# Kernel tuning notes

Hardware: AMD Instinct MI355X
Metric: run time of the kernel (lower is better)

Reference implementation:

```python
import jax, jax.numpy as jnp
import numpy as np

N_NODES = 50000
N_EDGES = 800000
IN_DIM = 128
HID = 128
N_GRAPHS = 1024


def gcn_conv(x, W, b, src, dst, n_nodes):
    # PyG GCNConv: add self-loops, symmetric normalization, aggregate at dst, then bias.
    loop = jnp.arange(n_nodes, dtype=src.dtype)
    s = jnp.concatenate([src, loop])
    d = jnp.concatenate([dst, loop])
    deg = jax.ops.segment_sum(jnp.ones_like(d, dtype=x.dtype), d, num_segments=n_nodes)
    dinv = jnp.where(deg > 0, deg ** -0.5, 0.0)
    norm = dinv[s] * dinv[d]                      # [E+N]
    h = x @ W                                     # [N, out]
    msg = h[s] * norm[:, None]                    # gather + scale
    out = jax.ops.segment_sum(msg, d, num_segments=n_nodes)  # scatter-add
    return out + b


def setup_inputs() -> dict:
    key = jax.random.key(0)
    ks = jax.random.split(key, 10)
    x = jax.random.normal(ks[0], (N_NODES, IN_DIM), dtype=jnp.float32)
    src = jax.random.randint(ks[1], (N_EDGES,), 0, N_NODES, dtype=jnp.int32)
    dst = jax.random.randint(ks[2], (N_EDGES,), 0, N_NODES, dtype=jnp.int32)
    batch = jnp.sort(jax.random.randint(ks[3], (N_NODES,), 0, N_GRAPHS, dtype=jnp.int32))
    sc1 = 1.0 / np.sqrt(IN_DIM)
    sc2 = 1.0 / np.sqrt(HID)
    W1 = jax.random.uniform(ks[4], (IN_DIM, HID), jnp.float32, -sc1, sc1)
    b1 = jnp.zeros((HID,), jnp.float32)
    W2 = jax.random.uniform(ks[5], (HID, HID), jnp.float32, -sc2, sc2)
    b2 = jnp.zeros((HID,), jnp.float32)
    Wlin = jax.random.uniform(ks[6], (HID, 1), jnp.float32, -sc2, sc2)
    blin = jnp.zeros((1,), jnp.float32)
    return {"x": x, "src": src, "dst": dst, "batch": batch, "n_graphs": N_GRAPHS,
            "W1": W1, "b1": b1, "W2": W2, "b2": b2, "Wlin": Wlin, "blin": blin}


def reference(x, src, dst, batch, n_graphs, W1, b1, W2, b2, Wlin, blin):
    n = x.shape[0]
    h = jax.nn.relu(gcn_conv(x, W1, b1, src, dst, n))
    h = jax.nn.relu(gcn_conv(h, W2, b2, src, dst, n))
    # global_mean_pool over graph assignment
    summed = jax.ops.segment_sum(h, batch, num_segments=n_graphs)
    cnt = jax.ops.segment_sum(jnp.ones((n,), h.dtype), batch, num_segments=n_graphs)
    pooled = summed / jnp.maximum(cnt, 1.0)[:, None]
    return (pooled @ Wlin + blin).reshape(-1)
```

## Files before the change

kernel.cpp:

```cpp
#include <hip/hip_runtime.h>
#include <hip/hip_bf16.h>

#define DIM 128
typedef unsigned int u32;

typedef __attribute__((ext_vector_type(8))) short bf16x8;
typedef __attribute__((ext_vector_type(4))) float f32x4;
typedef __attribute__((ext_vector_type(2))) float f32x2;

__device__ __forceinline__ u32 pack_bf16x2(float a, float b) {
    u32 ua = __float_as_uint(a), ub = __float_as_uint(b);
    ua = (ua + 0x7FFFu + ((ua >> 16) & 1u)) >> 16;
    ub = (ub + 0x7FFFu + ((ub >> 16) & 1u)) >> 16;
    return ua | (ub << 16);
}
__device__ __forceinline__ float2 unpack_bf16x2(u32 h) {
    return make_float2(__uint_as_float(h << 16), __uint_as_float(h & 0xFFFF0000u));
}

#if __has_builtin(__builtin_amdgcn_cvt_pk_f32_fp8) && __has_builtin(__builtin_amdgcn_cvt_pk_fp8_f32)
#define FP8_HW 1
#endif

__device__ __forceinline__ void dec4(float* d, u32 w) {
#ifdef FP8_HW
    f32x2 a = __builtin_amdgcn_cvt_pk_f32_fp8((int)w, false);
    f32x2 b = __builtin_amdgcn_cvt_pk_f32_fp8((int)w, true);
    d[0] = a.x; d[1] = a.y; d[2] = b.x; d[3] = b.y;
#else
    #pragma unroll
    for (int i = 0; i < 4; ++i) {
        u32 v = (w >> (8 * i)) & 0xFFu;
        u32 s = v >> 7, e = (v >> 3) & 15u, m = v & 7u;
        float nv = __uint_as_float((s << 31) | ((e + 120u) << 23) | (m << 20));
        float sv = (s ? -1.f : 1.f) * (float)m * 0.001953125f;
        d[i] = e ? nv : sv;
    }
#endif
}

#ifndef FP8_HW
__device__ __forceinline__ u32 enc_byte(float f) {
    u32 s = __float_as_uint(f) >> 31;
    float af = fminf(fabsf(f), 448.f);
    u32 b;
    if (af >= 0.015625f) {
        u32 m = __float_as_uint(af);
        m = m + 0x0007FFFFu + ((m >> 20) & 1u);
        u32 fe = (m >> 23) - 120u;
        if (fe > 15u) b = (15u << 3) | 6u;
        else          b = (fe << 3) | ((m >> 20) & 7u);
    } else {
        b = (u32)rintf(af * 512.f);
    }
    return b | (s << 7);
}
#endif

template<bool HI>
__device__ __forceinline__ u32 enc_pair(float a, float b, u32 old) {
#ifdef FP8_HW
    return (u32)__builtin_amdgcn_cvt_pk_fp8_f32(a, b, (int)old, HI);
#else
    u32 p = enc_byte(a) | (enc_byte(b) << 8);
    return HI ? ((old & 0x0000FFFFu) | (p << 16)) : ((old & 0xFFFF0000u) | p);
#endif
}

__device__ __forceinline__ void addrow8(float* acc, uint2 r) {
    float d[4];
    dec4(d, r.x);
    acc[0] += d[0]; acc[1] += d[1]; acc[2] += d[2]; acc[3] += d[3];
    dec4(d, r.y);
    acc[4] += d[0]; acc[5] += d[1]; acc[6] += d[2]; acc[7] += d[3];
}

__global__ void count_rank(int* __restrict__ deg, const int* __restrict__ dst,
                           int* __restrict__ rank, int* __restrict__ total, int E)
{
    int e = blockIdx.x * blockDim.x + threadIdx.x;
    if (e == 0) *total = 0;
    if (e < E) rank[e] = atomicAdd(&deg[dst[e]], 1);
}

__global__ __launch_bounds__(256) void alloc_offsets(
    const int* __restrict__ deg, int* __restrict__ start, int* __restrict__ endp,
    float* __restrict__ dinv, int* __restrict__ total,
    int* __restrict__ csr, int N,
    float* __restrict__ sums, float* __restrict__ cnt, int G,
    u32* __restrict__ B0, u32* __restrict__ B1)
{
    int i = blockIdx.x * blockDim.x + threadIdx.x;
    int lane = threadIdx.x & 63;
    if (i < G) { sums[i] = 0.f; cnt[i] = 0.f; }
    if (i < 32) {
        B0[(size_t)N * 32 + i] = 0u;
        B1[(size_t)N * 32 + i] = 0u;
    }
    int d  = (i < N) ? deg[i] : 0;
    int d4 = (d + 3) & ~3;
    int pre = d4;
    #pragma unroll
    for (int off = 1; off < 64; off <<= 1) {
        int v = __shfl_up(pre, off, 64);
        if (lane >= off) pre += v;
    }
    int waveTot = __shfl(pre, 63, 64);
    int base = 0;
    if (lane == 63) base = atomicAdd(total, waveTot);
    base = __shfl(base, 63, 64);
    if (i < N) {
        int st = base + pre - d4;
        start[i] = st;
        endp[i]  = st + d4;
        dinv[i]  = rsqrtf((float)(d + 1));
        for (int p = d; p < d4; ++p)
            csr[st + p] = N;
    }
}

__device__ __forceinline__ void gemm_body0(
    const float* __restrict__ X, const float* __restrict__ W,
    const float* __restrict__ dinv, u32* __restrict__ Y, int N,
    int tile0, int tstride)
{
    __shared__ u32   Abuf[16][68];
    __shared__ float Dbuf[16][132];

    const int t    = threadIdx.x;
    const int grp  = t >> 4;
    const int gl   = t & 15;
    const int lane = t & 63;
    const int wv   = t >> 6;
    const int lrow = lane & 15;
    const int lhi  = lane >> 4;

    bf16x8 bfr[2][4];
    {
        const float* wp = W + (size_t)(lhi * 8) * DIM + wv * 32 + lrow;
        #pragma unroll
        for (int nt = 0; nt < 2; ++nt)
            #pragma unroll
            for (int kc = 0; kc < 4; ++kc) {
                const float* p = wp + (size_t)(kc * 32) * DIM + nt * 16;
                union { u32 u[4]; bf16x8 v; } tmp;
                #pragma unroll
                for (int e = 0; e < 4; ++e)
                    tmp.u[e] = pack_bf16x2(p[(size_t)(2 * e) * DIM],
                                           p[(size_t)(2 * e + 1) * DIM]);
                bfr[nt][kc] = tmp.v;
            }
    }

    const int ntiles = (N + 15) >> 4;
    for (int tile = tile0; tile < ntiles; tile += tstride) {
        const int node = tile * 16 + grp;
        const bool valid = node < N;

        float4 a0 = make_float4(0.f, 0.f, 0.f, 0.f);
        float4 a1 = make_float4(0.f, 0.f, 0.f, 0.f);
        if (valid) {
            a0 = *(const float4*)&X[(size_t)node * DIM + gl * 8];
            a1 = *(const float4*)&X[(size_t)node * DIM + gl * 8 + 4];
        }
        uint4 pk;
        pk.x = pack_bf16x2(a0.x, a0.y);
        pk.y = pack_bf16x2(a0.z, a0.w);
        pk.z = pack_bf16x2(a1.x, a1.y);
        pk.w = pack_bf16x2(a1.z, a1.w);
        *(uint4*)&Abuf[grp][gl * 4] = pk;
        __syncthreads();

        f32x4 c0 = {0.f, 0.f, 0.f, 0.f};
        f32x4 c1 = {0.f, 0.f, 0.f, 0.f};
        #pragma unroll
        for (int kc = 0; kc < 4; ++kc) {
            bf16x8 afr = *(const bf16x8*)&Abuf[lrow][kc * 16 + lhi * 4];
            c0 = __builtin_amdgcn_mfma_f32_16x16x32_bf16(afr, bfr[0][kc], c0, 0, 0, 0);
            c1 = __builtin_amdgcn_mfma_f32_16x16x32_bf16(afr, bfr[1][kc], c1, 0, 0, 0);
        }
        #pragma unroll
        for (int r = 0; r < 4; ++r) {
            Dbuf[lhi * 4 + r][wv * 32 + lrow]      = c0[r];
            Dbuf[lhi * 4 + r][wv * 32 + 16 + lrow] = c1[r];
        }
        __syncthreads();

        if (valid) {
            float dnp = 16.f * dinv[node];
            float4 o0 = *(const float4*)&Dbuf[grp][gl * 8];
            float4 o1 = *(const float4*)&Dbuf[grp][gl * 8 + 4];
            u32 lo = enc_pair<false>(dnp * o0.x, dnp * o0.y, 0u);
            lo     = enc_pair<true >(dnp * o0.z, dnp * o0.w, lo);
            u32 hi = enc_pair<false>(dnp * o1.x, dnp * o1.y, 0u);
            hi     = enc_pair<true >(dnp * o1.z, dnp * o1.w, hi);
            *(uint2*)&Y[(size_t)node * 32 + gl * 2] = make_uint2(lo, hi);
        }
    }
}

__global__ __launch_bounds__(256) void scatter_gemm1(
    const float* __restrict__ x, const float* __restrict__ W1,
    const float* __restrict__ dinv, u32* __restrict__ Y, int N, int gblocks,
    const int* __restrict__ src, const int* __restrict__ dst,
    const int* __restrict__ rank, const int* __restrict__ start,
    int* __restrict__ csr, int E)
{
    if ((int)blockIdx.x < gblocks) {
        gemm_body0(x, W1, dinv, Y, N, blockIdx.x, gblocks);
    } else {
        int e = ((int)blockIdx.x - gblocks) * 256 + threadIdx.x;
        if (e < E) {
            int d = dst[e];
            csr[start[d] + rank[e]] = src[e];
        }
    }
}

__device__ __forceinline__ void gather_core8(
    const u32* __restrict__ Hl, const int* __restrict__ csr,
    int st, int en_pad, float* acc)
{
    int j = st;
    for (; j + 8 <= en_pad; j += 8) {
        int4 sa = *(const int4*)&csr[j];
        int4 sb = *(const int4*)&csr[j + 4];
        uint2 r0 = *(const uint2*)&Hl[(size_t)sa.x * 32];
        uint2 r1 = *(const uint2*)&Hl[(size_t)sa.y * 32];
        uint2 r2 = *(const uint2*)&Hl[(size_t)sa.z * 32];
        uint2 r3 = *(const uint2*)&Hl[(size_t)sa.w * 32];
        uint2 r4 = *(const uint2*)&Hl[(size_t)sb.x * 32];
        uint2 r5 = *(const uint2*)&Hl[(size_t)sb.y * 32];
        uint2 r6 = *(const uint2*)&Hl[(size_t)sb.z * 32];
        uint2 r7 = *(const uint2*)&Hl[(size_t)sb.w * 32];
        addrow8(acc, r0); addrow8(acc, r1); addrow8(acc, r2); addrow8(acc, r3);
        addrow8(acc, r4); addrow8(acc, r5); addrow8(acc, r6); addrow8(acc, r7);
    }
    if (j < en_pad) {
        int4 sa = *(const int4*)&csr[j];
        uint2 r0 = *(const uint2*)&Hl[(size_t)sa.x * 32];
        uint2 r1 = *(const uint2*)&Hl[(size_t)sa.y * 32];
        uint2 r2 = *(const uint2*)&Hl[(size_t)sa.z * 32];
        uint2 r3 = *(const uint2*)&Hl[(size_t)sa.w * 32];
        addrow8(acc, r0); addrow8(acc, r1); addrow8(acc, r2); addrow8(acc, r3);
    }
}

__global__ __launch_bounds__(256) void gather_gemm(
    const u32* __restrict__ H, u32* __restrict__ O,
    const int* __restrict__ csr, const int* __restrict__ start,
    const int* __restrict__ endp, const float* __restrict__ dinv, int N,
    const float* __restrict__ b1, const float* __restrict__ W2)
{
    __shared__ u32   Abuf[16][68];
    __shared__ float Dbuf[16][132];

    const int t    = threadIdx.x;
    const int grp  = t >> 4;
    const int gl   = t & 15;
    const int node = blockIdx.x * 16 + grp;
    const bool valid = node < N;

    const int lane = t & 63;
    const int wv   = t >> 6;
    const int lrow = lane & 15;
    const int lhi  = lane >> 4;

    bf16x8 bfr[2][4];
    {
        const float* wp = W2 + (size_t)(lhi * 8) * DIM + wv * 32 + lrow;
        #pragma unroll
        for (int nt = 0; nt < 2; ++nt)
            #pragma unroll
            for (int kc = 0; kc < 4; ++kc) {
                const float* p = wp + (size_t)(kc * 32) * DIM + nt * 16;
                union { u32 u[4]; bf16x8 v; } tmp;
                #pragma unroll
                for (int e = 0; e < 4; ++e)
                    tmp.u[e] = pack_bf16x2(p[(size_t)(2 * e) * DIM],
                                           p[(size_t)(2 * e + 1) * DIM]);
                bfr[nt][kc] = tmp.v;
            }
    }

    float acc[8] = {0.f,0.f,0.f,0.f,0.f,0.f,0.f,0.f};
    float dn = 0.f;
    if (valid) {
        const u32* Hl = H + gl * 2;
        gather_core8(Hl, csr, start[node], endp[node], acc);
        addrow8(acc, *(const uint2*)&Hl[(size_t)node * 32]);
        dn = dinv[node] * 0.0625f;
    }

    {
        int f0 = gl * 8;
        float4 bA = *(const float4*)&b1[f0];
        float4 bB = *(const float4*)&b1[f0 + 4];
        float bb[8] = {bA.x,bA.y,bA.z,bA.w,bB.x,bB.y,bB.z,bB.w};
        float r[8];
        #pragma unroll
        for (int i = 0; i < 8; ++i)
            r[i] = fmaxf(fmaf(dn, acc[i], bb[i]), 0.f);
        uint4 pk;
        pk.x = pack_bf16x2(r[0], r[1]);
        pk.y = pack_bf16x2(r[2], r[3]);
        pk.z = pack_bf16x2(r[4], r[5]);
        pk.w = pack_bf16x2(r[6], r[7]);
        *(uint4*)&Abuf[grp][gl * 4] = pk;
    }
    __syncthreads();

    f32x4 c0 = {0.f, 0.f, 0.f, 0.f};
    f32x4 c1 = {0.f, 0.f, 0.f, 0.f};
    #pragma unroll
    for (int kc = 0; kc < 4; ++kc) {
        bf16x8 afr = *(const bf16x8*)&Abuf[lrow][kc * 16 + lhi * 4];
        c0 = __builtin_amdgcn_mfma_f32_16x16x32_bf16(afr, bfr[0][kc], c0, 0, 0, 0);
        c1 = __builtin_amdgcn_mfma_f32_16x16x32_bf16(afr, bfr[1][kc], c1, 0, 0, 0);
    }

    #pragma unroll
    for (int r = 0; r < 4; ++r) {
        Dbuf[lhi * 4 + r][wv * 32 + lrow]      = c0[r];
        Dbuf[lhi * 4 + r][wv * 32 + 16 + lrow] = c1[r];
    }
    __syncthreads();

    if (valid) {
        float dnp = 16.f * dinv[node];
        float4 o0 = *(const float4*)&Dbuf[grp][gl * 8];
        float4 o1 = *(const float4*)&Dbuf[grp][gl * 8 + 4];
        u32 lo = enc_pair<false>(dnp * o0.x, dnp * o0.y, 0u);
        lo     = enc_pair<true >(dnp * o0.z, dnp * o0.w, lo);
        u32 hi = enc_pair<false>(dnp * o1.x, dnp * o1.y, 0u);
        hi     = enc_pair<true >(dnp * o1.z, dnp * o1.w, hi);
        *(uint2*)&O[(size_t)node * 32 + gl * 2] = make_uint2(lo, hi);
    }
}

__global__ __launch_bounds__(256) void gather_pool(
    const u32* __restrict__ H,
    const int* __restrict__ csr, const int* __restrict__ start,
    const int* __restrict__ endp, const float* __restrict__ dinv, int N,
    const float* __restrict__ b2, const float* __restrict__ wlin,
    const int* __restrict__ batch, float* __restrict__ sums, float* __restrict__ cnt)
{
    const int grp  = threadIdx.x >> 4;
    const int gl   = threadIdx.x & 15;
    const int node = blockIdx.x * 16 + grp;
    if (node >= N) return;

    float acc[8] = {0.f,0.f,0.f,0.f,0.f,0.f,0.f,0.f};
    const u32* Hl = H + gl * 2;
    gather_core8(Hl, csr, start[node], endp[node], acc);
    addrow8(acc, *(const uint2*)&Hl[(size_t)node * 32]);
    float dn = dinv[node] * 0.0625f;

    int f0 = gl * 8;
    float v = 0.f;
    #pragma unroll
    for (int i = 0; i < 8; ++i)
        v += fmaxf(fmaf(dn, acc[i], b2[f0 + i]), 0.f) * wlin[f0 + i];
    #pragma unroll
    for (int m = 1; m <= 8; m <<= 1) v += __shfl_xor(v, m, 64);
    if (gl == 0) {
        int g = batch[node];
        unsafeAtomicAdd(&sums[g], v);
        unsafeAtomicAdd(&cnt[g], 1.0f);
    }
}

__global__ void final_kernel(const float* __restrict__ sums,
                             const float* __restrict__ cnt,
                             const float* __restrict__ blin,
                             float* __restrict__ out, int G)
{
    int g = blockIdx.x * blockDim.x + threadIdx.x;
    if (g < G) out[g] = sums[g] / fmaxf(cnt[g], 1.0f) + blin[0];
}


extern "C" void kernel_launch(void* const* d_in, const int* in_sizes, int n_in,
                              void* d_out, int out_size, void* d_ws, size_t ws_size,
                              hipStream_t stream)
{
    const float* x    = (const float*)d_in[0];
    const int*   src  = (const int*)d_in[1];
    const int*   dst  = (const int*)d_in[2];
    const int*   batch= (const int*)d_in[3];
    const float* W1   = (const float*)d_in[5];
    const float* b1   = (const float*)d_in[6];
    const float* W2   = (const float*)d_in[7];
    const float* b2   = (const float*)d_in[8];
    const float* wlin = (const float*)d_in[9];
    const float* blin = (const float*)d_in[10];
    float* out = (float*)d_out;

    const int N = in_sizes[0] / DIM;
    const int E = in_sizes[1];
    const int G = out_size;
    const size_t E_pad = (size_t)E + 4 * (size_t)N;

    u32*   B0    = (u32*)d_ws;
    u32*   B1    = B0 + (size_t)(N + 1) * 32;
    float* dinv  = (float*)(B1 + (size_t)(N + 1) * 32);
    float* sums  = dinv + N;
    float* cnt   = sums + G;
    int*   deg_c = (int*)(cnt + G);
    int*   start = deg_c + N;
    int*   endp  = start + N;
    int*   rank  = endp + N;
    int*   csr   = rank + E;
    int*   total = csr + E_pad;
    size_t need_bytes = ((size_t)(total + 1) - (size_t)d_ws);
    if (ws_size < need_bytes) return;

    const int eblocks  = (E + 255) / 256;
    const int g4blocks = (N + 15) / 16;
    const int g1blocks = g4blocks < 1024 ? g4blocks : 1024;

    (void)hipMemsetAsync(deg_c, 0, sizeof(int) * (size_t)N, stream);
    count_rank<<<eblocks, 256, 0, stream>>>(deg_c, dst, rank, total, E);
    alloc_offsets<<<(N + 255) / 256, 256, 0, stream>>>(deg_c, start, endp,
                                                       dinv, total, csr, N,
                                                       sums, cnt, G, B0, B1);
    scatter_gemm1<<<g1blocks + eblocks, 256, 0, stream>>>(x, W1, dinv, B0, N,
                                                          g1blocks, src, dst,
                                                          rank, start, csr, E);
    gather_gemm<<<g4blocks, 256, 0, stream>>>(B0, B1, csr, start, endp, dinv,
                                              N, b1, W2);
    gather_pool<<<g4blocks, 256, 0, stream>>>(B1, csr, start, endp, dinv, N,
                                              b2, wlin, batch, sums, cnt);
    final_kernel<<<(G + 255) / 256, 256, 0, stream>>>(sums, cnt, blin, out, G);
}
```

Measured before the change: 245.2 us.

## Gather 16 fp8 features per thread and prefetch next CSR indices

The gather kernels now use 8 threads per node instead of 16. Each thread loads 16 fp8 features per neighbor as one 16-byte load, and each block covers 32 nodes. The gather loop is restructured to prefetch the next 8 CSR indices while the current neighbor rows are being loaded. The GEMM stage runs two MFMA halves over the 32-node tile. The goal is fewer, wider memory transactions and less index-load latency, at the cost of twice the accumulator registers and a halved thread count per node.

```diff
diff --git a/kernel.cpp b/kernel.cpp
--- a/kernel.cpp
+++ b/kernel.cpp
@@ -67,12 +67,16 @@
 #endif
 }
 
-__device__ __forceinline__ void addrow8(float* acc, uint2 r) {
+__device__ __forceinline__ void addrow16(float* acc, uint4 r) {
     float d[4];
     dec4(d, r.x);
-    acc[0] += d[0]; acc[1] += d[1]; acc[2] += d[2]; acc[3] += d[3];
+    acc[0]  += d[0]; acc[1]  += d[1]; acc[2]  += d[2]; acc[3]  += d[3];
     dec4(d, r.y);
-    acc[4] += d[0]; acc[5] += d[1]; acc[6] += d[2]; acc[7] += d[3];
+    acc[4]  += d[0]; acc[5]  += d[1]; acc[6]  += d[2]; acc[7]  += d[3];
+    dec4(d, r.z);
+    acc[8]  += d[0]; acc[9]  += d[1]; acc[10] += d[2]; acc[11] += d[3];
+    dec4(d, r.w);
+    acc[12] += d[0]; acc[13] += d[1]; acc[14] += d[2]; acc[15] += d[3];
 }
 
 __global__ void count_rank(int* __restrict__ deg, const int* __restrict__ dst,
@@ -217,32 +221,47 @@
     }
 }
 
-__device__ __forceinline__ void gather_core8(
+__device__ __forceinline__ void gather_core16(
     const u32* __restrict__ Hl, const int* __restrict__ csr,
-    int st, int en_pad, float* acc)
+    int st, int en, float* acc)
 {
     int j = st;
-    for (; j + 8 <= en_pad; j += 8) {
+    if (j + 8 <= en) {
         int4 sa = *(const int4*)&csr[j];
         int4 sb = *(const int4*)&csr[j + 4];
-        uint2 r0 = *(const uint2*)&Hl[(size_t)sa.x * 32];
-        uint2 r1 = *(const uint2*)&Hl[(size_t)sa.y * 32];
-        uint2 r2 = *(const uint2*)&Hl[(size_t)sa.z * 32];
-        uint2 r3 = *(const uint2*)&Hl[(size_t)sa.w * 32];
-        uint2 r4 = *(const uint2*)&Hl[(size_t)sb.x * 32];
-        uint2 r5 = *(const uint2*)&Hl[(size_t)sb.y * 32];
-        uint2 r6 = *(const uint2*)&Hl[(size_t)sb.z * 32];
-        uint2 r7 = *(const uint2*)&Hl[(size_t)sb.w * 32];
-        addrow8(acc, r0); addrow8(acc, r1); addrow8(acc, r2); addrow8(acc, r3);
-        addrow8(acc, r4); addrow8(acc, r5); addrow8(acc, r6); addrow8(acc, r7);
-    }
-    if (j < en_pad) {
+        while (true) {
+            int jn = j + 8;
+            bool next8 = (jn + 8 <= en);
+            int4 na, nb;
+            if (next8) {
+                na = *(const int4*)&csr[jn];
+                nb = *(const int4*)&csr[jn + 4];
+            }
+            uint4 r0 = *(const uint4*)&Hl[(size_t)sa.x * 32];
+            uint4 r1 = *(const uint4*)&Hl[(size_t)sa.y * 32];
+            uint4 r2 = *(const uint4*)&Hl[(size_t)sa.z * 32];
+            uint4 r3 = *(const uint4*)&Hl[(size_t)sa.w * 32];
+            uint4 r4 = *(const uint4*)&Hl[(size_t)sb.x * 32];
+            uint4 r5 = *(const uint4*)&Hl[(size_t)sb.y * 32];
+            uint4 r6 = *(const uint4*)&Hl[(size_t)sb.z * 32];
+            uint4 r7 = *(const uint4*)&Hl[(size_t)sb.w * 32];
+            addrow16(acc, r0); addrow16(acc, r1);
+            addrow16(acc, r2); addrow16(acc, r3);
+            addrow16(acc, r4); addrow16(acc, r5);
+            addrow16(acc, r6); addrow16(acc, r7);
+            j = jn;
+            if (!next8) break;
+            sa = na; sb = nb;
+        }
+    }
+    if (j < en) {
         int4 sa = *(const int4*)&csr[j];
-        uint2 r0 = *(const uint2*)&Hl[(size_t)sa.x * 32];
-        uint2 r1 = *(const uint2*)&Hl[(size_t)sa.y * 32];
-        uint2 r2 = *(const uint2*)&Hl[(size_t)sa.z * 32];
-        uint2 r3 = *(const uint2*)&Hl[(size_t)sa.w * 32];
-        addrow8(acc, r0); addrow8(acc, r1); addrow8(acc, r2); addrow8(acc, r3);
+        uint4 r0 = *(const uint4*)&Hl[(size_t)sa.x * 32];
+        uint4 r1 = *(const uint4*)&Hl[(size_t)sa.y * 32];
+        uint4 r2 = *(const uint4*)&Hl[(size_t)sa.z * 32];
+        uint4 r3 = *(const uint4*)&Hl[(size_t)sa.w * 32];
+        addrow16(acc, r0); addrow16(acc, r1);
+        addrow16(acc, r2); addrow16(acc, r3);
     }
 }
 
@@ -252,13 +271,13 @@
     const int* __restrict__ endp, const float* __restrict__ dinv, int N,
     const float* __restrict__ b1, const float* __restrict__ W2)
 {
-    __shared__ u32   Abuf[16][68];
-    __shared__ float Dbuf[16][132];
+    __shared__ u32   Abuf[32][68];
+    __shared__ float Dbuf[32][132];
 
     const int t    = threadIdx.x;
-    const int grp  = t >> 4;
-    const int gl   = t & 15;
-    const int node = blockIdx.x * 16 + grp;
+    const int grp  = t >> 3;
+    const int gl   = t & 7;
+    const int node = blockIdx.x * 32 + grp;
     const bool valid = node < N;
 
     const int lane = t & 63;
@@ -283,58 +302,75 @@
             }
     }
 
-    float acc[8] = {0.f,0.f,0.f,0.f,0.f,0.f,0.f,0.f};
+    float acc[16];
+    #pragma unroll
+    for (int i = 0; i < 16; ++i) acc[i] = 0.f;
     float dn = 0.f;
     if (valid) {
-        const u32* Hl = H + gl * 2;
-        gather_core8(Hl, csr, start[node], endp[node], acc);
-        addrow8(acc, *(const uint2*)&Hl[(size_t)node * 32]);
+        const u32* Hl = H + gl * 4;
+        gather_core16(Hl, csr, start[node], endp[node], acc);
+        addrow16(acc, *(const uint4*)&Hl[(size_t)node * 32]);
         dn = dinv[node] * 0.0625f;
     }
 
     {
-        int f0 = gl * 8;
-        float4 bA = *(const float4*)&b1[f0];
-        float4 bB = *(const float4*)&b1[f0 + 4];
-        float bb[8] = {bA.x,bA.y,bA.z,bA.w,bB.x,bB.y,bB.z,bB.w};
-        float r[8];
-        #pragma unroll
-        for (int i = 0; i < 8; ++i)
-            r[i] = fmaxf(fmaf(dn, acc[i], bb[i]), 0.f);
-        uint4 pk;
-        pk.x = pack_bf16x2(r[0], r[1]);
-        pk.y = pack_bf16x2(r[2], r[3]);
-        pk.z = pack_bf16x2(r[4], r[5]);
-        pk.w = pack_bf16x2(r[6], r[7]);
-        *(uint4*)&Abuf[grp][gl * 4] = pk;
+        int f0 = gl * 16;
+        float r[16];
+        #pragma unroll
+        for (int i = 0; i < 16; i += 4) {
+            float4 bb = *(const float4*)&b1[f0 + i];
+            r[i]     = fmaxf(fmaf(dn, acc[i],     bb.x), 0.f);
+            r[i + 1] = fmaxf(fmaf(dn, acc[i + 1], bb.y), 0.f);
+            r[i + 2] = fmaxf(fmaf(dn, acc[i + 2], bb.z), 0.f);
+            r[i + 3] = fmaxf(fmaf(dn, acc[i + 3], bb.w), 0.f);
+        }
+        uint4 p0, p1;
+        p0.x = pack_bf16x2(r[0],  r[1]);
+        p0.y = pack_bf16x2(r[2],  r[3]);
+        p0.z = pack_bf16x2(r[4],  r[5]);
+        p0.w = pack_bf16x2(r[6],  r[7]);
+        p1.x = pack_bf16x2(r[8],  r[9]);
+        p1.y = pack_bf16x2(r[10], r[11]);
+        p1.z = pack_bf16x2(r[12], r[13]);
+        p1.w = pack_bf16x2(r[14], r[15]);
+        *(uint4*)&Abuf[grp][gl * 8]     = p0;
+        *(uint4*)&Abuf[grp][gl * 8 + 4] = p1;
     }
     __syncthreads();
 
-    f32x4 c0 = {0.f, 0.f, 0.f, 0.f};
-    f32x4 c1 = {0.f, 0.f, 0.f, 0.f};
-    #pragma unroll
-    for (int kc = 0; kc < 4; ++kc) {
-        bf16x8 afr = *(const bf16x8*)&Abuf[lrow][kc * 16 + lhi * 4];
-        c0 = __builtin_amdgcn_mfma_f32_16x16x32_bf16(afr, bfr[0][kc], c0, 0, 0, 0);
-        c1 = __builtin_amdgcn_mfma_f32_16x16x32_bf16(afr, bfr[1][kc], c1, 0, 0, 0);
-    }
-
-    #pragma unroll
-    for (int r = 0; r < 4; ++r) {
-        Dbuf[lhi * 4 + r][wv * 32 + lrow]      = c0[r];
-        Dbuf[lhi * 4 + r][wv * 32 + 16 + lrow] = c1[r];
+    #pragma unroll
+    for (int half = 0; half < 2; ++half) {
+        f32x4 c0 = {0.f, 0.f, 0.f, 0.f};
+        f32x4 c1 = {0.f, 0.f, 0.f, 0.f};
+        #pragma unroll
+        for (int kc = 0; kc < 4; ++kc) {
+            bf16x8 afr = *(const bf16x8*)&Abuf[half * 16 + lrow][kc * 16 + lhi * 4];
+            c0 = __builtin_amdgcn_mfma_f32_16x16x32_bf16(afr, bfr[0][kc], c0, 0, 0, 0);
+            c1 = __builtin_amdgcn_mfma_f32_16x16x32_bf16(afr, bfr[1][kc], c1, 0, 0, 0);
+        }
+        #pragma unroll
+        for (int r = 0; r < 4; ++r) {
+            Dbuf[half * 16 + lhi * 4 + r][wv * 32 + lrow]      = c0[r];
+            Dbuf[half * 16 + lhi * 4 + r][wv * 32 + 16 + lrow] = c1[r];
+        }
     }
     __syncthreads();
 
     if (valid) {
         float dnp = 16.f * dinv[node];
-        float4 o0 = *(const float4*)&Dbuf[grp][gl * 8];
-        float4 o1 = *(const float4*)&Dbuf[grp][gl * 8 + 4];
-        u32 lo = enc_pair<false>(dnp * o0.x, dnp * o0.y, 0u);
-        lo     = enc_pair<true >(dnp * o0.z, dnp * o0.w, lo);
-        u32 hi = enc_pair<false>(dnp * o1.x, dnp * o1.y, 0u);
-        hi     = enc_pair<true >(dnp * o1.z, dnp * o1.w, hi);
-        *(uint2*)&O[(size_t)node * 32 + gl * 2] = make_uint2(lo, hi);
+        float o[16];
+        #pragma unroll
+        for (int i = 0; i < 16; ++i) o[i] = Dbuf[grp][gl * 16 + i];
+        uint4 ov;
+        ov.x = enc_pair<true>(dnp * o[2],  dnp * o[3],
+               enc_pair<false>(dnp * o[0],  dnp * o[1],  0u));
+        ov.y = enc_pair<true>(dnp * o[6],  dnp * o[7],
+               enc_pair<false>(dnp * o[4],  dnp * o[5],  0u));
+        ov.z = enc_pair<true>(dnp * o[10], dnp * o[11],
+               enc_pair<false>(dnp * o[8],  dnp * o[9],  0u));
+        ov.w = enc_pair<true>(dnp * o[14], dnp * o[15],
+               enc_pair<false>(dnp * o[12], dnp * o[13], 0u));
+        *(uint4*)&O[(size_t)node * 32 + gl * 4] = ov;
     }
 }
 
@@ -345,24 +381,33 @@
     const float* __restrict__ b2, const float* __restrict__ wlin,
     const int* __restrict__ batch, float* __restrict__ sums, float* __restrict__ cnt)
 {
-    const int grp  = threadIdx.x >> 4;
-    const int gl   = threadIdx.x & 15;
-    const int node = blockIdx.x * 16 + grp;
+    const int grp  = threadIdx.x >> 3;
+    const int gl   = threadIdx.x & 7;
+    const int node = blockIdx.x * 32 + grp;
     if (node >= N) return;
 
-    float acc[8] = {0.f,0.f,0.f,0.f,0.f,0.f,0.f,0.f};
-    const u32* Hl = H + gl * 2;
-    gather_core8(Hl, csr, start[node], endp[node], acc);
-    addrow8(acc, *(const uint2*)&Hl[(size_t)node * 32]);
+    float acc[16];
+    #pragma unroll
+    for (int i = 0; i < 16; ++i) acc[i] = 0.f;
+    const u32* Hl = H + gl * 4;
+    gather_core16(Hl, csr, start[node], endp[node], acc);
+    addrow16(acc, *(const uint4*)&Hl[(size_t)node * 32]);
     float dn = dinv[node] * 0.0625f;
 
-    int f0 = gl * 8;
+    int f0 = gl * 16;
     float v = 0.f;
     #pragma unroll
-    for (int i = 0; i < 8; ++i)
-        v += fmaxf(fmaf(dn, acc[i], b2[f0 + i]), 0.f) * wlin[f0 + i];
-    #pragma unroll
-    for (int m = 1; m <= 8; m <<= 1) v += __shfl_xor(v, m, 64);
+    for (int i = 0; i < 16; i += 4) {
+        float4 bb = *(const float4*)&b2[f0 + i];
+        float4 ww = *(const float4*)&wlin[f0 + i];
+        v += fmaxf(fmaf(dn, acc[i],     bb.x), 0.f) * ww.x;
+        v += fmaxf(fmaf(dn, acc[i + 1], bb.y), 0.f) * ww.y;
+        v += fmaxf(fmaf(dn, acc[i + 2], bb.z), 0.f) * ww.z;
+        v += fmaxf(fmaf(dn, acc[i + 3], bb.w), 0.f) * ww.w;
+    }
+    v += __shfl_xor(v, 1, 64);
+    v += __shfl_xor(v, 2, 64);
+    v += __shfl_xor(v, 4, 64);
     if (gl == 0) {
         int g = batch[node];
         unsafeAtomicAdd(&sums[g], v);
@@ -418,6 +463,7 @@
     const int eblocks  = (E + 255) / 256;
     const int g4blocks = (N + 15) / 16;
     const int g1blocks = g4blocks < 1024 ? g4blocks : 1024;
+    const int g32blocks = (N + 31) / 32;
 
     (void)hipMemsetAsync(deg_c, 0, sizeof(int) * (size_t)N, stream);
     count_rank<<<eblocks, 256, 0, stream>>>(deg_c, dst, rank, total, E);
@@ -427,9 +473,9 @@
     scatter_gemm1<<<g1blocks + eblocks, 256, 0, stream>>>(x, W1, dinv, B0, N,
                                                           g1blocks, src, dst,
                                                           rank, start, csr, E);
-    gather_gemm<<<g4blocks, 256, 0, stream>>>(B0, B1, csr, start, endp, dinv,
-                                              N, b1, W2);
-    gather_pool<<<g4blocks, 256, 0, stream>>>(B1, csr, start, endp, dinv, N,
-                                              b2, wlin, batch, sums, cnt);
+    gather_gemm<<<g32blocks, 256, 0, stream>>>(B0, B1, csr, start, endp, dinv,
+                                               N, b1, W2);
+    gather_pool<<<g32blocks, 256, 0, stream>>>(B1, csr, start, endp, dinv, N,
+                                               b2, wlin, batch, sums, cnt);
     final_kernel<<<(G + 255) / 256, 256, 0, stream>>>(sums, cnt, blin, out, G);
 }
```

New measurement: 237.9 us. 3.0% less time.
